# Kernel optimization log

Measured on AMD Instinct MI355X. Metric: run time of the kernel, lower is better.

## Reference

```python
import jax, jax.numpy as jnp
import numpy as np

B, S, E, H, DH = 4, 2048, 2048, 16, 256  # DH = mlp hidden (d_hid)
HD = E // H  # per-head dim = 128
EPS = 1e-5

def _ln(x, w, b):
    m = jnp.mean(x, axis=-1, keepdims=True)
    v = jnp.mean(jnp.square(x - m), axis=-1, keepdims=True)
    return (x - m) * jax.lax.rsqrt(v + EPS) * w + b

def setup_inputs() -> dict:
    key = jax.random.key(0)
    ks = jax.random.split(key, 10)
    s = 0.02
    return {
        "x": jax.random.normal(ks[0], (B, S, E), jnp.float32),
        "attention_mask": jax.random.randint(ks[1], (B, S), 0, 2, jnp.int32),
        "ln1_w": jnp.ones((E,), jnp.float32),
        "ln1_b": jnp.zeros((E,), jnp.float32),
        "in_proj_w": jax.random.normal(ks[2], (3 * E, E), jnp.float32) * s,
        "in_proj_b": jnp.zeros((3 * E,), jnp.float32),
        "out_proj_w": jax.random.normal(ks[3], (E, E), jnp.float32) * s,
        "out_proj_b": jnp.zeros((E,), jnp.float32),
        "ln2_w": jnp.ones((E,), jnp.float32),
        "ln2_b": jnp.zeros((E,), jnp.float32),
        "mlp_w1": jax.random.normal(ks[4], (DH, E), jnp.float32) * s,
        "mlp_b1": jnp.zeros((DH,), jnp.float32),
        "mlp_w2": jax.random.normal(ks[5], (E, DH), jnp.float32) * s,
        "mlp_b2": jnp.zeros((E,), jnp.float32),
    }

def reference(x, attention_mask, ln1_w, ln1_b, in_proj_w, in_proj_b,
              out_proj_w, out_proj_b, ln2_w, ln2_b, mlp_w1, mlp_b1, mlp_w2, mlp_b2):
    h = _ln(x, ln1_w, ln1_b)
    qkv = h @ in_proj_w.T + in_proj_b  # [B,S,3E]
    q, k, v = jnp.split(qkv, 3, axis=-1)
    q = q.reshape(B, S, H, HD).transpose(0, 2, 1, 3) / jnp.sqrt(jnp.float32(HD))
    k = k.reshape(B, S, H, HD).transpose(0, 2, 1, 3)
    v = v.reshape(B, S, H, HD).transpose(0, 2, 1, 3)
    scores = jnp.einsum("bhqd,bhkd->bhqk", q, k)
    # Faithful to source: FLOAT attn_mask of +1.0 on strictly-upper triangle (additive),
    # NOT -inf; key_padding_mask positions do get -inf.
    causal_add = jnp.triu(jnp.ones((S, S), jnp.float32), k=1)
    scores = scores + causal_add
    pad = (attention_mask == 0)  # True = padded key
    scores = jnp.where(pad[:, None, None, :], jnp.float32(-jnp.inf), scores)
    attn = jax.nn.softmax(scores, axis=-1)
    ctx = jnp.einsum("bhqk,bhkd->bhqd", attn, v)
    ctx = ctx.transpose(0, 2, 1, 3).reshape(B, S, E)
    x = x + ctx @ out_proj_w.T + out_proj_b
    h2 = _ln(x, ln2_w, ln2_b)
    mlp = jax.nn.relu(h2 @ mlp_w1.T + mlp_b1) @ mlp_w2.T + mlp_b2
    return x + mlp
```

## Files before the change

### kernel.cpp

```cpp
#include <hip/hip_runtime.h>

typedef __attribute__((ext_vector_type(8))) short short8;
typedef __attribute__((ext_vector_type(4))) float f32x4;
typedef __attribute__((ext_vector_type(16))) float f32x16;

typedef __attribute__((address_space(1))) const void gas1_t;
typedef __attribute__((address_space(3))) void las3_t;
#define GLL16(g, l) __builtin_amdgcn_global_load_lds((gas1_t*)(g), (las3_t*)(l), 16, 0, 0)

__device__ inline unsigned short f2bf(float f) {
  union { float f; unsigned int u; } v; v.f = f;
  unsigned int r = v.u + 0x7FFFu + ((v.u >> 16) & 1u);
  return (unsigned short)(r >> 16);
}

__device__ inline float exp2_fast(float x) {
  float r; asm("v_exp_f32 %0, %1" : "=v"(r) : "v"(x)); return r;
}

__device__ inline void vmwait(int n) {
  if (n == 6)      asm volatile("s_waitcnt vmcnt(6)" ::: "memory");
  else             asm volatile("s_waitcnt vmcnt(0)" ::: "memory");
}

__global__ __launch_bounds__(256) void ln_kernel(const float* __restrict__ x,
                                                 const float* __restrict__ w,
                                                 const float* __restrict__ bia,
                                                 unsigned short* __restrict__ out) {
  const int row = blockIdx.x;
  const int tid = threadIdx.x;
  const float* xr = x + (size_t)row * 2048;
  float4 a = *(const float4*)(xr + tid * 8);
  float4 b = *(const float4*)(xr + tid * 8 + 4);
  float s  = a.x + a.y + a.z + a.w + b.x + b.y + b.z + b.w;
  float s2 = a.x*a.x + a.y*a.y + a.z*a.z + a.w*a.w + b.x*b.x + b.y*b.y + b.z*b.z + b.w*b.w;
  #pragma unroll
  for (int off = 1; off < 64; off <<= 1) {
    s  += __shfl_xor(s, off);
    s2 += __shfl_xor(s2, off);
  }
  __shared__ float red[8];
  if ((tid & 63) == 0) { red[tid >> 6] = s; red[4 + (tid >> 6)] = s2; }
  __syncthreads();
  s  = red[0] + red[1] + red[2] + red[3];
  s2 = red[4] + red[5] + red[6] + red[7];
  const float mean = s * (1.f / 2048.f);
  const float var  = s2 * (1.f / 2048.f) - mean * mean;
  const float rstd = rsqrtf(var + 1e-5f);
  float4 wa = *(const float4*)(w + tid * 8), wb = *(const float4*)(w + tid * 8 + 4);
  float4 ba = *(const float4*)(bia + tid * 8), bb = *(const float4*)(bia + tid * 8 + 4);
  short8 o;
  o[0] = (short)f2bf((a.x - mean) * rstd * wa.x + ba.x);
  o[1] = (short)f2bf((a.y - mean) * rstd * wa.y + ba.y);
  o[2] = (short)f2bf((a.z - mean) * rstd * wa.z + ba.z);
  o[3] = (short)f2bf((a.w - mean) * rstd * wa.w + ba.w);
  o[4] = (short)f2bf((b.x - mean) * rstd * wb.x + bb.x);
  o[5] = (short)f2bf((b.y - mean) * rstd * wb.y + bb.y);
  o[6] = (short)f2bf((b.z - mean) * rstd * wb.z + bb.z);
  o[7] = (short)f2bf((b.w - mean) * rstd * wb.w + bb.w);
  *(short8*)(out + (size_t)row * 2048 + tid * 8) = o;
}

__global__ __launch_bounds__(256) void conv_kernel(const float* __restrict__ in,
                                                   unsigned short* __restrict__ out, int n) {
  size_t idx = ((size_t)blockIdx.x * 256 + threadIdx.x) * 8;
  if (idx >= (size_t)n) return;
  float4 a = *(const float4*)(in + idx);
  float4 b = *(const float4*)(in + idx + 4);
  short8 o;
  o[0] = (short)f2bf(a.x); o[1] = (short)f2bf(a.y);
  o[2] = (short)f2bf(a.z); o[3] = (short)f2bf(a.w);
  o[4] = (short)f2bf(b.x); o[5] = (short)f2bf(b.y);
  o[6] = (short)f2bf(b.z); o[7] = (short)f2bf(b.w);
  *(short8*)(out + idx) = o;
}

template <int MODE>
__global__ __launch_bounds__(256) void gemm_bt(const unsigned short* __restrict__ A,
                                               const unsigned short* __restrict__ Bw,
                                               const float* __restrict__ bias,
                                               const float* __restrict__ res,
                                               void* __restrict__ outp,
                                               void* __restrict__ outp2,
                                               int M, int N, int K) {
  __shared__ unsigned short As[128 * 64];
  __shared__ unsigned short Bs[128 * 64];
  const int tid = threadIdx.x;
  const int l = tid & 63, wv = tid >> 6;
  const int l15 = l & 15, l4 = l >> 4;
  const int wr = wv >> 1, wc = wv & 1;
  const int nx = gridDim.x;
  const int nwg = nx * gridDim.y;
  const int bidlin = blockIdx.y * nx + blockIdx.x;
  const int cpx = nwg >> 3;
  const int swz = (bidlin & 7) * cpx + (bidlin >> 3);
  const int m0 = (swz / nx) * 128, n0 = (swz % nx) * 128;

  f32x4 acc[4][4] = {};
  for (int k0 = 0; k0 < K; k0 += 64) {
    __syncthreads();
    #pragma unroll
    for (int i = 0; i < 4; ++i) {
      int e = i * 2048 + tid * 8;
      int r = e >> 6;
      int c = (e ^ ((r & 7) << 3)) & 63;
      GLL16(A + (size_t)(m0 + r) * K + k0 + c, As + e);
      GLL16(Bw + (size_t)(n0 + r) * K + k0 + c, Bs + e);
    }
    __syncthreads();
    #pragma unroll
    for (int kk = 0; kk < 64; kk += 32) {
      short8 af[4], bfr[4];
      #pragma unroll
      for (int m = 0; m < 4; ++m) {
        int r = wr * 64 + m * 16 + l15;
        int byt = (r * 128 + (kk + l4 * 8) * 2) ^ ((r & 7) << 4);
        af[m] = *(const short8*)((const char*)As + byt);
      }
      #pragma unroll
      for (int n = 0; n < 4; ++n) {
        int r = wc * 64 + n * 16 + l15;
        int byt = (r * 128 + (kk + l4 * 8) * 2) ^ ((r & 7) << 4);
        bfr[n] = *(const short8*)((const char*)Bs + byt);
      }
      #pragma unroll
      for (int m = 0; m < 4; ++m)
        #pragma unroll
        for (int n = 0; n < 4; ++n)
          acc[m][n] = __builtin_amdgcn_mfma_f32_16x16x32_bf16(af[m], bfr[n], acc[m][n], 0, 0, 0);
    }
  }
  #pragma unroll
  for (int m = 0; m < 4; ++m) {
    #pragma unroll
    for (int n = 0; n < 4; ++n) {
      #pragma unroll
      for (int r = 0; r < 4; ++r) {
        int row = m0 + wr * 64 + m * 16 + l4 * 4 + r;
        int col = n0 + wc * 64 + n * 16 + l15;
        float v = acc[m][n][r] + bias[col];
        if (MODE == 1) {
          ((unsigned short*)outp)[(size_t)row * N + col] = f2bf(v > 0.f ? v : 0.f);
        } else {
          ((float*)outp)[(size_t)row * N + col] = res[(size_t)row * N + col] + v;
        }
      }
    }
  }
}

template <int MODE>
__global__ __launch_bounds__(512, 2) void gemm8(const unsigned short* __restrict__ A,
                                                const unsigned short* __restrict__ Bw,
                                                const float* __restrict__ bias,
                                                const float* __restrict__ res,
                                                const int* __restrict__ amask,
                                                void* __restrict__ outp,
                                                int M, int N, int K) {
  __shared__ char LA[2][2][16384];
  __shared__ char LB[2][2][16384];
  const int tid = threadIdx.x;
  const int l = tid & 63, wv = tid >> 6;
  const int l15 = l & 15, l4 = l >> 4;
  const int wr = wv >> 2, wc = wv & 3;
  const int wch = wc >> 1, wcl = wc & 1;
  const int nx = gridDim.x;
  const int nwg = nx * gridDim.y;
  const int bidlin = blockIdx.y * nx + blockIdx.x;
  const int cpx = nwg >> 3;
  const int swz = (bidlin & 7) * cpx + (bidlin >> 3);
  const int m0 = (swz / nx) * 256, n0 = (swz % nx) * 256;

  const int srow = tid >> 3;
  const int scol = ((tid & 7) ^ (srow & 7)) * 8;

#define STG_A(x, h) { const unsigned short* bp = A + (size_t)(m0 + (h) * 128) * K + (x) * 64; \
    GLL16(bp + (size_t)srow * K + scol, &LA[(x) & 1][h][tid * 16]); \
    GLL16(bp + (size_t)(srow + 64) * K + scol, &LA[(x) & 1][h][8192 + tid * 16]); }
#define STG_B(x, h) { const unsigned short* bp = Bw + (size_t)(n0 + (h) * 128) * K + (x) * 64; \
    GLL16(bp + (size_t)srow * K + scol, &LB[(x) & 1][h][tid * 16]); \
    GLL16(bp + (size_t)(srow + 64) * K + scol, &LB[(x) & 1][h][8192 + tid * 16]); }

#define FOFF(r, kh) ((r) * 128 + (((((kh) * 4 + l4)) ^ ((r) & 7)) << 4))

  f32x4 acc[8][4] = {};
  const int NT = K >> 6;

  STG_A(0, 0); STG_A(0, 1); STG_B(0, 0); STG_B(0, 1);
  STG_B(1, 0); STG_B(1, 1); STG_A(1, 0);
  vmwait(6);
  __builtin_amdgcn_s_barrier();

#define MFMAK(mh, kh) \
    __builtin_amdgcn_s_setprio(1); \
    _Pragma("unroll") for (int f = 0; f < 4; ++f) \
      _Pragma("unroll") for (int n = 0; n < 4; ++n) { \
        if (MODE == 3) \
          acc[(mh) * 4 + f][n] = __builtin_amdgcn_mfma_f32_16x16x32_bf16( \
              bfr[kh][n], af[kh][f], acc[(mh) * 4 + f][n], 0, 0, 0); \
        else \
          acc[(mh) * 4 + f][n] = __builtin_amdgcn_mfma_f32_16x16x32_bf16( \
              af[kh][f], bfr[kh][n], acc[(mh) * 4 + f][n], 0, 0, 0); \
      } \
    __builtin_amdgcn_s_setprio(0);

  for (int t = 0; t < NT; ++t) {
    const char* Ab = LA[t & 1][wr];
    const char* Bb = LB[t & 1][wch];
    short8 af[2][4], bfr[2][4];
    #pragma unroll
    for (int f = 0; f < 4; ++f) {
      bfr[0][f] = *(const short8*)(Bb + FOFF(wcl * 64 + f * 16 + l15, 0));
      af[0][f]  = *(const short8*)(Ab + FOFF(f * 16 + l15, 0));
    }
    __builtin_amdgcn_sched_barrier(0);
    #pragma unroll
    for (int f = 0; f < 4; ++f) {
      bfr[1][f] = *(const short8*)(Bb + FOFF(wcl * 64 + f * 16 + l15, 1));
      af[1][f]  = *(const short8*)(Ab + FOFF(f * 16 + l15, 1));
    }
    if (t + 1 < NT) STG_A(t + 1, 1);
    __builtin_amdgcn_s_barrier();
    asm volatile("s_waitcnt lgkmcnt(8)" ::: "memory");
    __builtin_amdgcn_sched_barrier(0);
    MFMAK(0, 0);
    asm volatile("s_waitcnt lgkmcnt(0)" ::: "memory");
    __builtin_amdgcn_sched_barrier(0);
    MFMAK(0, 1);
    __builtin_amdgcn_s_barrier();
    #pragma unroll
    for (int f = 0; f < 4; ++f)
      af[0][f] = *(const short8*)(Ab + FOFF(64 + f * 16 + l15, 0));
    __builtin_amdgcn_sched_barrier(0);
    #pragma unroll
    for (int f = 0; f < 4; ++f)
      af[1][f] = *(const short8*)(Ab + FOFF(64 + f * 16 + l15, 1));
    if (t + 2 < NT) { STG_B(t + 2, 0); STG_B(t + 2, 1); STG_A(t + 2, 0); }
    __builtin_amdgcn_s_barrier();
    asm volatile("s_waitcnt lgkmcnt(4)" ::: "memory");
    __builtin_amdgcn_sched_barrier(0);
    MFMAK(1, 0);
    asm volatile("s_waitcnt lgkmcnt(0)" ::: "memory");
    __builtin_amdgcn_sched_barrier(0);
    MFMAK(1, 1);
    vmwait(t >= NT - 2 ? 0 : 6);
    __builtin_amdgcn_s_barrier();
  }
#undef MFMAK
#undef FOFF
#undef STG_A
#undef STG_B

  #pragma unroll
  for (int mf = 0; mf < 8; ++mf) {
    int tokenv = 0, amv = 1;
    if (MODE == 3) {
      tokenv = m0 + wr * 128 + mf * 16 + l15;
      amv = amask[tokenv];
    }
    #pragma unroll
    for (int nf = 0; nf < 4; ++nf) {
      #pragma unroll
      for (int r = 0; r < 4; ++r) {
        if (MODE == 3) {
          int vcol = n0 + wc * 64 + nf * 16 + l4 * 4 + r;
          float v = (amv != 0) ? (acc[mf][nf][r] + bias[vcol]) : 0.f;
          int hh = vcol >> 7, d = vcol & 127;
          int bb = tokenv >> 11;
          ((unsigned short*)outp)[((size_t)(bb * 16 + hh) * 128 + d) * 2048 +
                                  (tokenv & 2047)] = f2bf(v);
        } else {
          int row = m0 + wr * 128 + mf * 16 + l4 * 4 + r;
          int col = n0 + wc * 64 + nf * 16 + l15;
          float v = acc[mf][nf][r] + bias[col];
          if (MODE == 0) {
            ((unsigned short*)outp)[(size_t)row * 4096 + col] = f2bf(v);
          } else {
            ((float*)outp)[(size_t)row * N + col] = res[(size_t)row * N + col] + v;
          }
        }
      }
    }
  }
}

__global__ __launch_bounds__(256) void attn_kernel(const unsigned short* __restrict__ qk,
                                                   const unsigned short* __restrict__ vT,
                                                   const int* __restrict__ amask,
                                                   unsigned short* __restrict__ ctx) {
  __shared__ unsigned short Ks[2][4096];
  __shared__ unsigned short Vs[2][4096];
  __shared__ unsigned short validbf[2048];

  const int lin = blockIdx.y * 16 + blockIdx.x;
  const int swzb = (lin & 7) * 128 + (lin >> 3);
  const int qt = swzb & 15, bh = swzb >> 4;
  const int b = bh >> 4, h = bh & 15;
  const int tid = threadIdx.x;
  const int wv = tid >> 6, l = tid & 63;
  const int l31 = l & 31, hi = l >> 5;
  const int q0w = qt * 128 + wv * 32;
  const float SC2 = 0.08838834764831845f * 1.4426950408889634f;
  const float L2E = 1.4426950408889634f;
  const float MF  = 10.0f;

  int kinv[2], vinv[2];
  #pragma unroll
  for (int c = 0; c < 2; ++c) {
    int e = c * 2048 + tid * 8;
    int key = e >> 7, d0 = e & 127;
    kinv[c] = key * 4096 + 2048 + h * 128 + (d0 ^ ((key & 7) << 3));
    int d = e >> 5, kchunk = ((e >> 3) & 3) ^ ((d & 6) >> 1);
    vinv[c] = d * 2048 + kchunk * 8;
  }
  const unsigned short* kb0 = qk + (size_t)(b * 2048) * 4096;
  const unsigned short* vb0 = vT + (size_t)(b * 16 + h) * (128 * 2048);
  const int* mrow = amask + b * 2048;

  {
    int i8 = tid * 8;
    short8 vv;
    #pragma unroll
    for (int j = 0; j < 8; ++j) vv[j] = (short)(mrow[i8 + j] ? 0x3F80 : 0);
    *(short8*)&validbf[i8] = vv;
  }

  short8 qf[8];
  {
    const unsigned short* qp = qk + (size_t)(b * 2048 + q0w + l31) * 4096 + h * 128 + hi * 8;
    #pragma unroll
    for (int c = 0; c < 8; ++c) qf[c] = *(const short8*)(qp + c * 16);
  }

  f32x16 o[4] = {};
  f32x16 ol = {};

  #pragma unroll
  for (int c = 0; c < 2; ++c) {
    GLL16(kb0 + kinv[c], &Ks[0][c * 2048 + tid * 8]);
    GLL16(vb0 + vinv[c], &Vs[0][c * 2048 + tid * 8]);
  }
  __syncthreads();

  for (int kt = 0; kt < 2048; kt += 32) {
    const int cur = (kt >> 5) & 1;
    if (kt + 32 < 2048) {
      #pragma unroll
      for (int c = 0; c < 2; ++c) {
        GLL16(kb0 + (size_t)(kt + 32) * 4096 + kinv[c], &Ks[cur ^ 1][c * 2048 + tid * 8]);
        GLL16(vb0 + (kt + 32) + vinv[c], &Vs[cur ^ 1][c * 2048 + tid * 8]);
      }
    }

    f32x16 sacc = {};
    __builtin_amdgcn_s_setprio(1);
    #pragma unroll
    for (int c = 0; c < 8; ++c) {
      short8 kf = *(const short8*)((const char*)Ks[cur] +
                   ((l31 * 256 + c * 32 + hi * 16) ^ ((l31 & 7) << 4)));
      sacc = __builtin_amdgcn_mfma_f32_32x32x16_bf16(kf, qf[c], sacc, 0, 0, 0);
    }
    __builtin_amdgcn_s_setprio(0);

    const int Dq = q0w + l31 - kt - 4 * hi;
    float p[16];
    if (kt > q0w + 31) {
      #pragma unroll
      for (int i = 0; i < 16; ++i) p[i] = sacc[i] * SC2 + (L2E - MF);
    } else if (kt + 31 <= q0w) {
      #pragma unroll
      for (int i = 0; i < 16; ++i) p[i] = sacc[i] * SC2 - MF;
    } else {
      #pragma unroll
      for (int i = 0; i < 16; ++i) {
        const int ci = (i & 3) + 8 * (i >> 2);
        p[i] = sacc[i] * SC2 + ((ci > Dq) ? (L2E - MF) : -MF);
      }
    }
    #pragma unroll
    for (int i = 0; i < 16; ++i) p[i] = exp2_fast(p[i]);

#define CVTPK(dst, a, bsrc) asm("v_cvt_pk_bf16_f32 %0, %1, %2" : "=v"(dst) : "v"(a), "v"(bsrc))
#define PLSWAP(fst, snd) asm("v_permlane32_swap_b32 %0, %1" : "+v"(fst), "+v"(snd))
    unsigned x, x2, y, y2, u, u2, v, v2;
    CVTPK(x,  p[0],  p[1]);  CVTPK(x2, p[2],  p[3]);
    CVTPK(y,  p[4],  p[5]);  CVTPK(y2, p[6],  p[7]);
    CVTPK(u,  p[8],  p[9]);  CVTPK(u2, p[10], p[11]);
    CVTPK(v,  p[12], p[13]); CVTPK(v2, p[14], p[15]);
    PLSWAP(x, y);  PLSWAP(x2, y2);
    PLSWAP(u, v);  PLSWAP(u2, v2);
    union { unsigned w[4]; short8 s8; } P0, P1;
    P0.w[0] = x; P0.w[1] = x2; P0.w[2] = y; P0.w[3] = y2;
    P1.w[0] = u; P1.w[1] = u2; P1.w[2] = v; P1.w[3] = v2;
    short8 pa0 = P0.s8, pa1 = P1.s8;
#undef CVTPK
#undef PLSWAP

    short8 vm0 = *(const short8*)&validbf[kt + hi * 8];
    short8 vm1 = *(const short8*)&validbf[kt + 16 + hi * 8];

    __builtin_amdgcn_s_setprio(1);
    #pragma unroll
    for (int g = 0; g < 4; ++g) {
      int d = g * 32 + l31;
      int swzd = (d & 6) << 3;
      short8 vf0 = *(const short8*)((const char*)Vs[cur] + ((d * 64 + hi * 16) ^ swzd));
      o[g] = __builtin_amdgcn_mfma_f32_32x32x16_bf16(pa0, vf0, o[g], 0, 0, 0);
      short8 vf1 = *(const short8*)((const char*)Vs[cur] + ((d * 64 + 32 + hi * 16) ^ swzd));
      o[g] = __builtin_amdgcn_mfma_f32_32x32x16_bf16(pa1, vf1, o[g], 0, 0, 0);
    }
    ol = __builtin_amdgcn_mfma_f32_32x32x16_bf16(pa0, vm0, ol, 0, 0, 0);
    ol = __builtin_amdgcn_mfma_f32_32x32x16_bf16(pa1, vm1, ol, 0, 0, 0);
    __builtin_amdgcn_s_setprio(0);

    __syncthreads();
  }

  float inv[16];
  #pragma unroll
  for (int i = 0; i < 16; ++i) inv[i] = 1.0f / ol[i];
  #pragma unroll
  for (int g = 0; g < 4; ++g) {
    #pragma unroll
    for (int i = 0; i < 16; ++i) {
      int q = q0w + (i & 3) + 8 * (i >> 2) + 4 * hi;
      ctx[(size_t)(b * 2048 + q) * 2048 + h * 128 + g * 32 + l31] = f2bf(o[g][i] * inv[i]);
    }
  }
}

extern "C" void kernel_launch(void* const* d_in, const int* in_sizes, int n_in,
                              void* d_out, int out_size, void* d_ws, size_t ws_size,
                              hipStream_t stream) {
  (void)in_sizes; (void)n_in; (void)out_size; (void)ws_size;
  const float* x    = (const float*)d_in[0];
  const int*   am   = (const int*)d_in[1];
  const float* ln1w = (const float*)d_in[2];
  const float* ln1b = (const float*)d_in[3];
  const float* win  = (const float*)d_in[4];
  const float* bin  = (const float*)d_in[5];
  const float* wout = (const float*)d_in[6];
  const float* bout = (const float*)d_in[7];
  const float* ln2w = (const float*)d_in[8];
  const float* ln2b = (const float*)d_in[9];
  const float* w1   = (const float*)d_in[10];
  const float* b1   = (const float*)d_in[11];
  const float* w2   = (const float*)d_in[12];
  const float* b2   = (const float*)d_in[13];
  float* out = (float*)d_out;

  char* ws = (char*)d_ws;
  unsigned short* hbuf = (unsigned short*)ws;
  unsigned short* ctxb = (unsigned short*)ws;
  unsigned short* qkb  = (unsigned short*)(ws + (size_t)32 * 1048576);
  unsigned short* h2b  = (unsigned short*)(ws + (size_t)32 * 1048576);
  unsigned short* midb = (unsigned short*)(ws + (size_t)64 * 1048576);
  unsigned short* vTb  = (unsigned short*)(ws + (size_t)96 * 1048576);
  unsigned short* wbuf = (unsigned short*)(ws + (size_t)128 * 1048576);

  ln_kernel<<<dim3(8192), dim3(256), 0, stream>>>(x, ln1w, ln1b, hbuf);
  conv_kernel<<<dim3(6144), dim3(256), 0, stream>>>(win, wbuf, 12582912);
  gemm8<0><<<dim3(16, 32), dim3(512), 0, stream>>>(hbuf, wbuf, bin, (const float*)nullptr,
                                                   (const int*)nullptr, (void*)qkb,
                                                   8192, 4096, 2048);
  gemm8<3><<<dim3(8, 32), dim3(512), 0, stream>>>(hbuf, wbuf + (size_t)4096 * 2048,
                                                  bin + 4096, (const float*)nullptr,
                                                  am, (void*)vTb, 8192, 2048, 2048);
  attn_kernel<<<dim3(16, 64), dim3(256), 0, stream>>>(qkb, vTb, am, ctxb);
  conv_kernel<<<dim3(2048), dim3(256), 0, stream>>>(wout, wbuf, 4194304);
  gemm8<2><<<dim3(8, 32), dim3(512), 0, stream>>>(ctxb, wbuf, bout, x,
                                                  (const int*)nullptr, (void*)out,
                                                  8192, 2048, 2048);
  ln_kernel<<<dim3(8192), dim3(256), 0, stream>>>(out, ln2w, ln2b, h2b);
  conv_kernel<<<dim3(256), dim3(256), 0, stream>>>(w1, wbuf, 524288);
  gemm_bt<1><<<dim3(2, 64), dim3(256), 0, stream>>>(h2b, wbuf, b1, (const float*)nullptr,
                                                    (void*)midb, nullptr, 8192, 256, 2048);
  conv_kernel<<<dim3(256), dim3(256), 0, stream>>>(w2, wbuf, 524288);
  gemm8<2><<<dim3(8, 32), dim3(512), 0, stream>>>(midb, wbuf, b2, out,
                                                  (const int*)nullptr, (void*)out,
                                                  8192, 2048, 256);
}
```

Measured before the change: 584.3 us.

## Merge QK and V projection GEMMs into one launch; batch weight conversions

Combines the separate QK projection GEMM and the transposed-V projection GEMM into a single gemm8 launch over N=6144. Blocks covering the V columns take a swapped-operand MFMA path and write the masked, transposed V output to a second pointer. The three later weight conversions (out_proj, w1, w2) are also merged into one kernel writing a dedicated buffer. This removes launches and the tail of the smaller V GEMM, at the cost of a larger template with divergent per-block code paths.

```diff
diff --git a/kernel.cpp b/kernel.cpp
--- a/kernel.cpp
+++ b/kernel.cpp
@@ -75,6 +75,26 @@
   *(short8*)(out + idx) = o;
 }
 
+__global__ __launch_bounds__(256) void conv3_kernel(const float* __restrict__ wo,
+                                                    const float* __restrict__ w1,
+                                                    const float* __restrict__ w2,
+                                                    unsigned short* __restrict__ out) {
+  size_t idx = ((size_t)blockIdx.x * 256 + threadIdx.x) * 8;
+  if (idx >= 5242880) return;
+  const float* src;
+  if (idx < 4194304)      src = wo + idx;
+  else if (idx < 4718592) src = w1 + (idx - 4194304);
+  else                    src = w2 + (idx - 4718592);
+  float4 a = *(const float4*)(src);
+  float4 b = *(const float4*)(src + 4);
+  short8 o;
+  o[0] = (short)f2bf(a.x); o[1] = (short)f2bf(a.y);
+  o[2] = (short)f2bf(a.z); o[3] = (short)f2bf(a.w);
+  o[4] = (short)f2bf(b.x); o[5] = (short)f2bf(b.y);
+  o[6] = (short)f2bf(b.z); o[7] = (short)f2bf(b.w);
+  *(short8*)(out + idx) = o;
+}
+
 template <int MODE>
 __global__ __launch_bounds__(256) void gemm_bt(const unsigned short* __restrict__ A,
                                                const unsigned short* __restrict__ Bw,
@@ -156,6 +176,7 @@
                                                 const float* __restrict__ res,
                                                 const int* __restrict__ amask,
                                                 void* __restrict__ outp,
+                                                void* __restrict__ outp2,
                                                 int M, int N, int K) {
   __shared__ char LA[2][2][16384];
   __shared__ char LB[2][2][16384];
@@ -170,6 +191,7 @@
   const int cpx = nwg >> 3;
   const int swz = (bidlin & 7) * cpx + (bidlin >> 3);
   const int m0 = (swz / nx) * 256, n0 = (swz % nx) * 256;
+  const bool vblk = (MODE == 4) && (n0 >= 4096);
 
   const int srow = tid >> 3;
   const int scol = ((tid & 7) ^ (srow & 7)) * 8;
@@ -191,11 +213,11 @@
   vmwait(6);
   __builtin_amdgcn_s_barrier();
 
-#define MFMAK(mh, kh) \
+#define MFMAK(mh, kh, SW) \
     __builtin_amdgcn_s_setprio(1); \
     _Pragma("unroll") for (int f = 0; f < 4; ++f) \
       _Pragma("unroll") for (int n = 0; n < 4; ++n) { \
-        if (MODE == 3) \
+        if (SW) \
           acc[(mh) * 4 + f][n] = __builtin_amdgcn_mfma_f32_16x16x32_bf16( \
               bfr[kh][n], af[kh][f], acc[(mh) * 4 + f][n], 0, 0, 0); \
         else \
@@ -204,48 +226,52 @@
       } \
     __builtin_amdgcn_s_setprio(0);
 
-  for (int t = 0; t < NT; ++t) {
-    const char* Ab = LA[t & 1][wr];
-    const char* Bb = LB[t & 1][wch];
-    short8 af[2][4], bfr[2][4];
-    #pragma unroll
-    for (int f = 0; f < 4; ++f) {
-      bfr[0][f] = *(const short8*)(Bb + FOFF(wcl * 64 + f * 16 + l15, 0));
-      af[0][f]  = *(const short8*)(Ab + FOFF(f * 16 + l15, 0));
-    }
-    __builtin_amdgcn_sched_barrier(0);
-    #pragma unroll
-    for (int f = 0; f < 4; ++f) {
-      bfr[1][f] = *(const short8*)(Bb + FOFF(wcl * 64 + f * 16 + l15, 1));
-      af[1][f]  = *(const short8*)(Ab + FOFF(f * 16 + l15, 1));
-    }
-    if (t + 1 < NT) STG_A(t + 1, 1);
-    __builtin_amdgcn_s_barrier();
-    asm volatile("s_waitcnt lgkmcnt(8)" ::: "memory");
-    __builtin_amdgcn_sched_barrier(0);
-    MFMAK(0, 0);
-    asm volatile("s_waitcnt lgkmcnt(0)" ::: "memory");
-    __builtin_amdgcn_sched_barrier(0);
-    MFMAK(0, 1);
-    __builtin_amdgcn_s_barrier();
-    #pragma unroll
-    for (int f = 0; f < 4; ++f)
-      af[0][f] = *(const short8*)(Ab + FOFF(64 + f * 16 + l15, 0));
-    __builtin_amdgcn_sched_barrier(0);
-    #pragma unroll
-    for (int f = 0; f < 4; ++f)
-      af[1][f] = *(const short8*)(Ab + FOFF(64 + f * 16 + l15, 1));
-    if (t + 2 < NT) { STG_B(t + 2, 0); STG_B(t + 2, 1); STG_A(t + 2, 0); }
-    __builtin_amdgcn_s_barrier();
-    asm volatile("s_waitcnt lgkmcnt(4)" ::: "memory");
-    __builtin_amdgcn_sched_barrier(0);
-    MFMAK(1, 0);
-    asm volatile("s_waitcnt lgkmcnt(0)" ::: "memory");
-    __builtin_amdgcn_sched_barrier(0);
-    MFMAK(1, 1);
-    vmwait(t >= NT - 2 ? 0 : 6);
-    __builtin_amdgcn_s_barrier();
-  }
+#define KLOOP(SW) \
+  for (int t = 0; t < NT; ++t) { \
+    const char* Ab = LA[t & 1][wr]; \
+    const char* Bb = LB[t & 1][wch]; \
+    short8 af[2][4], bfr[2][4]; \
+    _Pragma("unroll") for (int f = 0; f < 4; ++f) { \
+      bfr[0][f] = *(const short8*)(Bb + FOFF(wcl * 64 + f * 16 + l15, 0)); \
+      af[0][f]  = *(const short8*)(Ab + FOFF(f * 16 + l15, 0)); \
+    } \
+    __builtin_amdgcn_sched_barrier(0); \
+    _Pragma("unroll") for (int f = 0; f < 4; ++f) { \
+      bfr[1][f] = *(const short8*)(Bb + FOFF(wcl * 64 + f * 16 + l15, 1)); \
+      af[1][f]  = *(const short8*)(Ab + FOFF(f * 16 + l15, 1)); \
+    } \
+    if (t + 1 < NT) STG_A(t + 1, 1); \
+    __builtin_amdgcn_s_barrier(); \
+    asm volatile("s_waitcnt lgkmcnt(8)" ::: "memory"); \
+    __builtin_amdgcn_sched_barrier(0); \
+    MFMAK(0, 0, SW); \
+    asm volatile("s_waitcnt lgkmcnt(0)" ::: "memory"); \
+    __builtin_amdgcn_sched_barrier(0); \
+    MFMAK(0, 1, SW); \
+    __builtin_amdgcn_s_barrier(); \
+    _Pragma("unroll") for (int f = 0; f < 4; ++f) \
+      af[0][f] = *(const short8*)(Ab + FOFF(64 + f * 16 + l15, 0)); \
+    __builtin_amdgcn_sched_barrier(0); \
+    _Pragma("unroll") for (int f = 0; f < 4; ++f) \
+      af[1][f] = *(const short8*)(Ab + FOFF(64 + f * 16 + l15, 1)); \
+    if (t + 2 < NT) { STG_B(t + 2, 0); STG_B(t + 2, 1); STG_A(t + 2, 0); } \
+    __builtin_amdgcn_s_barrier(); \
+    asm volatile("s_waitcnt lgkmcnt(4)" ::: "memory"); \
+    __builtin_amdgcn_sched_barrier(0); \
+    MFMAK(1, 0, SW); \
+    asm volatile("s_waitcnt lgkmcnt(0)" ::: "memory"); \
+    __builtin_amdgcn_sched_barrier(0); \
+    MFMAK(1, 1, SW); \
+    vmwait(t >= NT - 2 ? 0 : 6); \
+    __builtin_amdgcn_s_barrier(); \
+  }
+
+  if (MODE == 4) {
+    if (vblk) { KLOOP(1) } else { KLOOP(0) }
+  } else {
+    KLOOP(0)
+  }
+#undef KLOOP
 #undef MFMAK
 #undef FOFF
 #undef STG_A
@@ -254,30 +280,34 @@
   #pragma unroll
   for (int mf = 0; mf < 8; ++mf) {
     int tokenv = 0, amv = 1;
-    if (MODE == 3) {
+    if (MODE == 4) {
       tokenv = m0 + wr * 128 + mf * 16 + l15;
-      amv = amask[tokenv];
+      if (vblk) amv = amask[tokenv];
     }
     #pragma unroll
     for (int nf = 0; nf < 4; ++nf) {
       #pragma unroll
       for (int r = 0; r < 4; ++r) {
-        if (MODE == 3) {
-          int vcol = n0 + wc * 64 + nf * 16 + l4 * 4 + r;
-          float v = (amv != 0) ? (acc[mf][nf][r] + bias[vcol]) : 0.f;
-          int hh = vcol >> 7, d = vcol & 127;
-          int bb = tokenv >> 11;
-          ((unsigned short*)outp)[((size_t)(bb * 16 + hh) * 128 + d) * 2048 +
-                                  (tokenv & 2047)] = f2bf(v);
+        if (MODE == 4) {
+          if (vblk) {
+            int col = n0 + wc * 64 + nf * 16 + l4 * 4 + r;
+            float v = (amv != 0) ? (acc[mf][nf][r] + bias[col]) : 0.f;
+            int vcol = col - 4096;
+            int hh = vcol >> 7, d = vcol & 127;
+            int bb = tokenv >> 11;
+            ((unsigned short*)outp2)[((size_t)(bb * 16 + hh) * 128 + d) * 2048 +
+                                     (tokenv & 2047)] = f2bf(v);
+          } else {
+            int col = n0 + wc * 64 + nf * 16 + l15;
+            float v = acc[mf][nf][r] + bias[col];
+            int row = m0 + wr * 128 + mf * 16 + l4 * 4 + r;
+            ((unsigned short*)outp)[(size_t)row * 4096 + col] = f2bf(v);
+          }
         } else {
           int row = m0 + wr * 128 + mf * 16 + l4 * 4 + r;
           int col = n0 + wc * 64 + nf * 16 + l15;
           float v = acc[mf][nf][r] + bias[col];
-          if (MODE == 0) {
-            ((unsigned short*)outp)[(size_t)row * 4096 + col] = f2bf(v);
-          } else {
-            ((float*)outp)[(size_t)row * N + col] = res[(size_t)row * N + col] + v;
-          }
+          ((float*)outp)[(size_t)row * N + col] = res[(size_t)row * N + col] + v;
         }
       }
     }
@@ -450,33 +480,33 @@
   float* out = (float*)d_out;
 
   char* ws = (char*)d_ws;
-  unsigned short* hbuf = (unsigned short*)ws;
-  unsigned short* ctxb = (unsigned short*)ws;
-  unsigned short* qkb  = (unsigned short*)(ws + (size_t)32 * 1048576);
-  unsigned short* h2b  = (unsigned short*)(ws + (size_t)32 * 1048576);
-  unsigned short* midb = (unsigned short*)(ws + (size_t)64 * 1048576);
-  unsigned short* vTb  = (unsigned short*)(ws + (size_t)96 * 1048576);
-  unsigned short* wbuf = (unsigned short*)(ws + (size_t)128 * 1048576);
+  unsigned short* hbuf  = (unsigned short*)ws;
+  unsigned short* ctxb  = (unsigned short*)ws;
+  unsigned short* qkb   = (unsigned short*)(ws + (size_t)32 * 1048576);
+  unsigned short* h2b   = (unsigned short*)(ws + (size_t)32 * 1048576);
+  unsigned short* midb  = (unsigned short*)(ws + (size_t)64 * 1048576);
+  unsigned short* wbuf2 = (unsigned short*)(ws + (size_t)68 * 1048576);
+  unsigned short* vTb   = (unsigned short*)(ws + (size_t)96 * 1048576);
+  unsigned short* wbuf  = (unsigned short*)(ws + (size_t)128 * 1048576);
+
+  unsigned short* woutb = wbuf2;
+  unsigned short* w1b   = wbuf2 + 4194304;
+  unsigned short* w2b   = wbuf2 + 4718592;
 
   ln_kernel<<<dim3(8192), dim3(256), 0, stream>>>(x, ln1w, ln1b, hbuf);
   conv_kernel<<<dim3(6144), dim3(256), 0, stream>>>(win, wbuf, 12582912);
-  gemm8<0><<<dim3(16, 32), dim3(512), 0, stream>>>(hbuf, wbuf, bin, (const float*)nullptr,
-                                                   (const int*)nullptr, (void*)qkb,
-                                                   8192, 4096, 2048);
-  gemm8<3><<<dim3(8, 32), dim3(512), 0, stream>>>(hbuf, wbuf + (size_t)4096 * 2048,
-                                                  bin + 4096, (const float*)nullptr,
-                                                  am, (void*)vTb, 8192, 2048, 2048);
+  gemm8<4><<<dim3(24, 32), dim3(512), 0, stream>>>(hbuf, wbuf, bin, (const float*)nullptr,
+                                                   am, (void*)qkb, (void*)vTb,
+                                                   8192, 6144, 2048);
   attn_kernel<<<dim3(16, 64), dim3(256), 0, stream>>>(qkb, vTb, am, ctxb);
-  conv_kernel<<<dim3(2048), dim3(256), 0, stream>>>(wout, wbuf, 4194304);
-  gemm8<2><<<dim3(8, 32), dim3(512), 0, stream>>>(ctxb, wbuf, bout, x,
-                                                  (const int*)nullptr, (void*)out,
+  conv3_kernel<<<dim3(2560), dim3(256), 0, stream>>>(wout, w1, w2, wbuf2);
+  gemm8<2><<<dim3(8, 32), dim3(512), 0, stream>>>(ctxb, woutb, bout, x,
+                                                  (const int*)nullptr, (void*)out, nullptr,
                                                   8192, 2048, 2048);
   ln_kernel<<<dim3(8192), dim3(256), 0, stream>>>(out, ln2w, ln2b, h2b);
-  conv_kernel<<<dim3(256), dim3(256), 0, stream>>>(w1, wbuf, 524288);
-  gemm_bt<1><<<dim3(2, 64), dim3(256), 0, stream>>>(h2b, wbuf, b1, (const float*)nullptr,
+  gemm_bt<1><<<dim3(2, 64), dim3(256), 0, stream>>>(h2b, w1b, b1, (const float*)nullptr,
                                                     (void*)midb, nullptr, 8192, 256, 2048);
-  conv_kernel<<<dim3(256), dim3(256), 0, stream>>>(w2, wbuf, 524288);
-  gemm8<2><<<dim3(8, 32), dim3(512), 0, stream>>>(midb, wbuf, b2, out,
-                                                  (const int*)nullptr, (void*)out,
+  gemm8<2><<<dim3(8, 32), dim3(512), 0, stream>>>(midb, w2b, b2, out,
+                                                  (const int*)nullptr, (void*)out, nullptr,
                                                   8192, 2048, 256);
 }
```

Measured after the change: 613.9 us. +5.1%, slower.
